# Kernel optimization log

Measured on AMD Instinct MI355X. Metric: run time of the kernel, lower is better.

## Reference

```python
import jax, jax.numpy as jnp
import numpy as np

B, C, H, W = 8, 64, 256, 256  # H must equal W for the second matmul


def setup_inputs() -> dict:
    key = jax.random.key(0)
    kq, kk, kv = jax.random.split(key, 3)
    Q = jax.random.normal(kq, (B, C, H, W), dtype=jnp.float32)
    K = jax.random.normal(kk, (B, C, H, W), dtype=jnp.float32)
    V = jax.random.normal(kv, (B, C, H, W), dtype=jnp.float32)
    di = jnp.ones((1,), dtype=jnp.float32)  # learned scalar scale
    return {"Q": Q, "K": K, "V": V, "di": di}


def reference(Q, K, V, di):
    # similarity[b,c,i,k] = sum_w Q[b,c,i,w] * K[b,c,k,w], scaled by di
    sim = jnp.einsum('bciw,bckw->bcik', Q, K) * di[0]
    attn = jax.nn.softmax(sim, axis=-1)  # [B,C,H,H]
    # residual = attn @ V^T -> [B,C,H,H]; output is residual^T:
    # out[b,c,i,j] = sum_k attn[b,c,j,k] * V[b,c,i,k]
    out = jnp.einsum('bcjk,bcik->bcij', attn, V)
    return out
```

## Files before the change

### kernel.cpp

```cpp
#include <hip/hip_runtime.h>
#include <hip/hip_bf16.h>


typedef __attribute__((ext_vector_type(8))) _Float16 f16x8;
typedef __attribute__((ext_vector_type(4))) float f32x4;
typedef __attribute__((ext_vector_type(16))) float f32x16;

#define BARRIER() asm volatile("s_waitcnt lgkmcnt(0)\n\ts_barrier" ::: "memory")

__device__ __forceinline__ f32x4 mfma16h(f16x8 a, f16x8 b, f32x4 c) {
  return __builtin_amdgcn_mfma_f32_16x16x32_f16(a, b, c, 0, 0, 0);
}
__device__ __forceinline__ f32x16 mfma32h(f16x8 a, f16x8 b, f32x16 c) {
  return __builtin_amdgcn_mfma_f32_32x32x16_f16(a, b, c, 0, 0, 0);
}
__device__ __forceinline__ f16x8 cvt8(f32x4 a, f32x4 b) {
  f16x8 r;
  r[0] = (_Float16)a[0]; r[1] = (_Float16)a[1];
  r[2] = (_Float16)a[2]; r[3] = (_Float16)a[3];
  r[4] = (_Float16)b[0]; r[5] = (_Float16)b[1];
  r[6] = (_Float16)b[2]; r[7] = (_Float16)b[3];
  return r;
}
__device__ __forceinline__ int swz(int row, int byteCol) {
  return row * 512 + (byteCol ^ ((row & 15) << 4));
}

__global__ __launch_bounds__(512, 2) void attn_fused6(
    const float* __restrict__ Q, const float* __restrict__ K,
    const float* __restrict__ V, const float* __restrict__ di,
    float* __restrict__ out) {
  __shared__ short Kbuf[2][32 * 256];
  __shared__ short Abuf[128 * 256];
  short* Vlds = &Kbuf[0][0];

  const int t = threadIdx.x;
  const int lane = t & 63;
  const int wv = t >> 6;
  const int l15 = lane & 15;
  const int l4 = (lane >> 4) & 3;
  const int l31 = lane & 31;
  const int h5 = lane >> 5;

  const int bid = blockIdx.x;
  const int bc = (bid >> 4) * 8 + (bid & 7);
  const int j0 = ((bid >> 3) & 1) << 7;

  const float dival = di[0];
  const size_t base = (size_t)bc << 16;
  const float* Qs = Q + base;
  const float* Ks = K + base;
  const float* Vs = V + base;
  float* Os = out + base;

  const int sr = t >> 4;
  const int sc = (t & 15) << 4;

  f32x4 ka0, ka1, ka2, ka3, kb0, kb1, kb2, kb3;
  {
    const float* p = Ks + sr * 256 + sc;
    ka0 = *(const f32x4*)p;
    ka1 = *(const f32x4*)(p + 4);
    ka2 = *(const f32x4*)(p + 8);
    ka3 = *(const f32x4*)(p + 12);
    const float* q = p + 8192;
    kb0 = *(const f32x4*)q;
    kb1 = *(const f32x4*)(q + 4);
    kb2 = *(const f32x4*)(q + 8);
    kb3 = *(const f32x4*)(q + 12);
  }
  f16x8 qh[8];
  {
    const float* qrow = Qs + (size_t)(j0 + wv * 16 + l15) * 256 + 8 * l4;
#pragma unroll
    for (int s = 0; s < 8; ++s)
      qh[s] = cvt8(*(const f32x4*)(qrow + 32 * s),
                   *(const f32x4*)(qrow + 32 * s + 4));
  }

  f32x4 acc[16];
#pragma unroll
  for (int i = 0; i < 16; ++i) acc[i] = (f32x4){0.f, 0.f, 0.f, 0.f};

#pragma unroll
  for (int ch = 0; ch < 8; ++ch) {
    short* kb = Kbuf[ch & 1];
    if ((ch & 1) == 0) {
      *(f16x8*)((char*)kb + swz(sr, sc * 2)) = cvt8(ka0, ka1);
      *(f16x8*)((char*)kb + swz(sr, sc * 2 + 16)) = cvt8(ka2, ka3);
      if (ch < 6) {
        const float* p = Ks + (ch + 2) * 8192 + sr * 256 + sc;
        ka0 = *(const f32x4*)p;
        ka1 = *(const f32x4*)(p + 4);
        ka2 = *(const f32x4*)(p + 8);
        ka3 = *(const f32x4*)(p + 12);
      }
    } else {
      *(f16x8*)((char*)kb + swz(sr, sc * 2)) = cvt8(kb0, kb1);
      *(f16x8*)((char*)kb + swz(sr, sc * 2 + 16)) = cvt8(kb2, kb3);
      if (ch < 6) {
        const float* p = Ks + (ch + 2) * 8192 + sr * 256 + sc;
        kb0 = *(const f32x4*)p;
        kb1 = *(const f32x4*)(p + 4);
        kb2 = *(const f32x4*)(p + 8);
        kb3 = *(const f32x4*)(p + 12);
      }
    }
    BARRIER();
    __builtin_amdgcn_s_setprio(1);
#pragma unroll
    for (int kf = 0; kf < 2; ++kf) {
      const int kr = kf * 16 + l15;
      f32x4 a = acc[2 * ch + kf];
#pragma unroll
      for (int s = 0; s < 8; ++s) {
        f16x8 bh = *(const f16x8*)((const char*)kb + swz(kr, 64 * s + 16 * l4));
        a = mfma16h(qh[s], bh, a);
      }
      acc[2 * ch + kf] = a;
    }
    __builtin_amdgcn_s_setprio(0);
  }

  const int vr = t >> 3;
  const int vc = (t & 7) << 5;
  f32x4 va[8], vb[8];
  {
    const float* p = Vs + (size_t)vr * 256 + vc;
#pragma unroll
    for (int e = 0; e < 8; ++e) va[e] = *(const f32x4*)(p + 4 * e);
  }

  float mx[4] = {-1e30f, -1e30f, -1e30f, -1e30f};
#pragma unroll
  for (int idx = 0; idx < 16; ++idx)
#pragma unroll
    for (int r = 0; r < 4; ++r) {
      acc[idx][r] *= dival;
      mx[r] = fmaxf(mx[r], acc[idx][r]);
    }
#pragma unroll
  for (int o = 1; o <= 8; o <<= 1)
#pragma unroll
    for (int r = 0; r < 4; ++r) mx[r] = fmaxf(mx[r], __shfl_xor(mx[r], o));
  float sm[4] = {0.f, 0.f, 0.f, 0.f};
#pragma unroll
  for (int idx = 0; idx < 16; ++idx)
#pragma unroll
    for (int r = 0; r < 4; ++r) {
      acc[idx][r] = __expf(acc[idx][r] - mx[r]);
      sm[r] += acc[idx][r];
    }
#pragma unroll
  for (int o = 1; o <= 8; o <<= 1)
#pragma unroll
    for (int r = 0; r < 4; ++r) sm[r] += __shfl_xor(sm[r], o);
#pragma unroll
  for (int r = 0; r < 4; ++r) sm[r] = 1.0f / sm[r];
#pragma unroll
  for (int idx = 0; idx < 16; ++idx)
#pragma unroll
    for (int r = 0; r < 4; ++r) {
      const int row = wv * 16 + 4 * l4 + r;
      *(_Float16*)((char*)Abuf + swz(row, 2 * (idx * 16 + l15))) =
          (_Float16)(acc[idx][r] * sm[r]);
    }
  BARRIER();

  const int ih = wv >> 2;
  const int jg = (wv & 3) * 32;
  f16x8 pb[16];
#pragma unroll
  for (int kk = 0; kk < 16; ++kk)
    pb[kk] =
        *(const f16x8*)((const char*)Abuf + swz(jg + l31, 32 * kk + 16 * h5));

#pragma unroll
  for (int ci = 0; ci < 4; ++ci) {
    if ((ci & 1) == 0) {
#pragma unroll
      for (int e = 0; e < 4; ++e) {
        *(f16x8*)((char*)Vlds + swz(vr, vc * 2 + 16 * e)) =
            cvt8(va[2 * e], va[2 * e + 1]);
      }
      if (ci < 3) {
        const float* p = Vs + (size_t)((ci + 1) * 64 + vr) * 256 + vc;
#pragma unroll
        for (int e = 0; e < 8; ++e) vb[e] = *(const f32x4*)(p + 4 * e);
      }
    } else {
#pragma unroll
      for (int e = 0; e < 4; ++e) {
        *(f16x8*)((char*)Vlds + swz(vr, vc * 2 + 16 * e)) =
            cvt8(vb[2 * e], vb[2 * e + 1]);
      }
      if (ci < 3) {
        const float* p = Vs + (size_t)((ci + 1) * 64 + vr) * 256 + vc;
#pragma unroll
        for (int e = 0; e < 8; ++e) va[e] = *(const f32x4*)(p + 4 * e);
      }
    }
    BARRIER();
    __builtin_amdgcn_s_setprio(1);
    f32x16 o = {};
#pragma unroll
    for (int kk = 0; kk < 16; ++kk) {
      f16x8 vfrag = *(const f16x8*)((const char*)Vlds +
                                    swz(ih * 32 + l31, 32 * kk + 16 * h5));
      o = mfma32h(vfrag, pb[kk], o);
    }
    __builtin_amdgcn_s_setprio(0);
    const int rbase = ci * 64 + ih * 32 + 4 * h5;
    const int col = j0 + jg + l31;
#pragma unroll
    for (int reg = 0; reg < 16; ++reg) {
      const int rw = (reg & 3) + 8 * (reg >> 2);
      Os[(size_t)(rbase + rw) * 256 + col] = o[reg];
    }
    BARRIER();
  }
}

extern "C" void kernel_launch(void* const* d_in, const int* in_sizes, int n_in,
                              void* d_out, int out_size, void* d_ws,
                              size_t ws_size, hipStream_t stream) {
  const float* Q = (const float*)d_in[0];
  const float* K = (const float*)d_in[1];
  const float* V = (const float*)d_in[2];
  const float* di = (const float*)d_in[3];
  float* out = (float*)d_out;
  const int BC = in_sizes[0] / (256 * 256);
  hipLaunchKernelGGL(attn_fused6, dim3(BC * 2), dim3(512), 0, stream, Q, K, V,
                     di, out);
}
```

Measured before the change: 130.1 us.

## Split each block to 64 query rows with cross-wave softmax merge, raise occupancy

Each block now handles 64 output columns instead of 128, so the grid doubles and launch bounds allow 4 blocks per CU. Pairs of waves split the key dimension and combine partial max and sum through a small shared buffer. The second matmul moves from 32x32 to 16x16 MFMA tiles that read the attention matrix straight from LDS. This trades more parallelism and smaller LDS use for loading and converting K and V twice as often per output.

```diff
diff --git a/kernel.cpp b/kernel.cpp
--- a/kernel.cpp
+++ b/kernel.cpp
@@ -4,15 +4,11 @@
 
 typedef __attribute__((ext_vector_type(8))) _Float16 f16x8;
 typedef __attribute__((ext_vector_type(4))) float f32x4;
-typedef __attribute__((ext_vector_type(16))) float f32x16;
 
 #define BARRIER() asm volatile("s_waitcnt lgkmcnt(0)\n\ts_barrier" ::: "memory")
 
 __device__ __forceinline__ f32x4 mfma16h(f16x8 a, f16x8 b, f32x4 c) {
   return __builtin_amdgcn_mfma_f32_16x16x32_f16(a, b, c, 0, 0, 0);
-}
-__device__ __forceinline__ f32x16 mfma32h(f16x8 a, f16x8 b, f32x16 c) {
-  return __builtin_amdgcn_mfma_f32_32x32x16_f16(a, b, c, 0, 0, 0);
 }
 __device__ __forceinline__ f16x8 cvt8(f32x4 a, f32x4 b) {
   f16x8 r;
@@ -26,12 +22,13 @@
   return row * 512 + (byteCol ^ ((row & 15) << 4));
 }
 
-__global__ __launch_bounds__(512, 2) void attn_fused6(
+__global__ __launch_bounds__(512, 4) void attn_fused7(
     const float* __restrict__ Q, const float* __restrict__ K,
     const float* __restrict__ V, const float* __restrict__ di,
     float* __restrict__ out) {
   __shared__ short Kbuf[2][32 * 256];
-  __shared__ short Abuf[128 * 256];
+  __shared__ short Abuf[64 * 256];
+  __shared__ float pmps[64 * 4];
   short* Vlds = &Kbuf[0][0];
 
   const int t = threadIdx.x;
@@ -39,12 +36,10 @@
   const int wv = t >> 6;
   const int l15 = lane & 15;
   const int l4 = (lane >> 4) & 3;
-  const int l31 = lane & 31;
-  const int h5 = lane >> 5;
 
   const int bid = blockIdx.x;
-  const int bc = (bid >> 4) * 8 + (bid & 7);
-  const int j0 = ((bid >> 3) & 1) << 7;
+  const int bc = (bid >> 5) * 8 + (bid & 7);
+  const int j0 = ((bid >> 3) & 3) * 64;
 
   const float dival = di[0];
   const size_t base = (size_t)bc << 16;
@@ -52,6 +47,9 @@
   const float* Ks = K + base;
   const float* Vs = V + base;
   float* Os = out + base;
+
+  const int jt = wv >> 1;
+  const int kt = wv & 1;
 
   const int sr = t >> 4;
   const int sc = (t & 15) << 4;
@@ -71,16 +69,16 @@
   }
   f16x8 qh[8];
   {
-    const float* qrow = Qs + (size_t)(j0 + wv * 16 + l15) * 256 + 8 * l4;
+    const float* qrow = Qs + (size_t)(j0 + 16 * jt + l15) * 256 + 8 * l4;
 #pragma unroll
     for (int s = 0; s < 8; ++s)
       qh[s] = cvt8(*(const f32x4*)(qrow + 32 * s),
                    *(const f32x4*)(qrow + 32 * s + 4));
   }
 
-  f32x4 acc[16];
-#pragma unroll
-  for (int i = 0; i < 16; ++i) acc[i] = (f32x4){0.f, 0.f, 0.f, 0.f};
+  f32x4 acc[8];
+#pragma unroll
+  for (int i = 0; i < 8; ++i) acc[i] = (f32x4){0.f, 0.f, 0.f, 0.f};
 
 #pragma unroll
   for (int ch = 0; ch < 8; ++ch) {
@@ -108,17 +106,14 @@
     }
     BARRIER();
     __builtin_amdgcn_s_setprio(1);
-#pragma unroll
-    for (int kf = 0; kf < 2; ++kf) {
-      const int kr = kf * 16 + l15;
-      f32x4 a = acc[2 * ch + kf];
-#pragma unroll
-      for (int s = 0; s < 8; ++s) {
-        f16x8 bh = *(const f16x8*)((const char*)kb + swz(kr, 64 * s + 16 * l4));
-        a = mfma16h(qh[s], bh, a);
-      }
-      acc[2 * ch + kf] = a;
-    }
+    const int kr = 16 * kt + l15;
+    f32x4 a = acc[ch];
+#pragma unroll
+    for (int s = 0; s < 8; ++s) {
+      f16x8 bh = *(const f16x8*)((const char*)kb + swz(kr, 64 * s + 16 * l4));
+      a = mfma16h(qh[s], bh, a);
+    }
+    acc[ch] = a;
     __builtin_amdgcn_s_setprio(0);
   }
 
@@ -133,11 +128,11 @@
 
   float mx[4] = {-1e30f, -1e30f, -1e30f, -1e30f};
 #pragma unroll
-  for (int idx = 0; idx < 16; ++idx)
-#pragma unroll
-    for (int r = 0; r < 4; ++r) {
-      acc[idx][r] *= dival;
-      mx[r] = fmaxf(mx[r], acc[idx][r]);
+  for (int ch = 0; ch < 8; ++ch)
+#pragma unroll
+    for (int r = 0; r < 4; ++r) {
+      acc[ch][r] *= dival;
+      mx[r] = fmaxf(mx[r], acc[ch][r]);
     }
 #pragma unroll
   for (int o = 1; o <= 8; o <<= 1)
@@ -145,44 +140,50 @@
     for (int r = 0; r < 4; ++r) mx[r] = fmaxf(mx[r], __shfl_xor(mx[r], o));
   float sm[4] = {0.f, 0.f, 0.f, 0.f};
 #pragma unroll
-  for (int idx = 0; idx < 16; ++idx)
-#pragma unroll
-    for (int r = 0; r < 4; ++r) {
-      acc[idx][r] = __expf(acc[idx][r] - mx[r]);
-      sm[r] += acc[idx][r];
+  for (int ch = 0; ch < 8; ++ch)
+#pragma unroll
+    for (int r = 0; r < 4; ++r) {
+      acc[ch][r] = __expf(acc[ch][r] - mx[r]);
+      sm[r] += acc[ch][r];
     }
 #pragma unroll
   for (int o = 1; o <= 8; o <<= 1)
 #pragma unroll
     for (int r = 0; r < 4; ++r) sm[r] += __shfl_xor(sm[r], o);
-#pragma unroll
-  for (int r = 0; r < 4; ++r) sm[r] = 1.0f / sm[r];
-#pragma unroll
-  for (int idx = 0; idx < 16; ++idx)
-#pragma unroll
-    for (int r = 0; r < 4; ++r) {
-      const int row = wv * 16 + 4 * l4 + r;
-      *(_Float16*)((char*)Abuf + swz(row, 2 * (idx * 16 + l15))) =
-          (_Float16)(acc[idx][r] * sm[r]);
-    }
+  if (l15 == 0) {
+#pragma unroll
+    for (int r = 0; r < 4; ++r) {
+      const int row = 16 * jt + 4 * l4 + r;
+      pmps[row * 4 + 2 * kt] = mx[r];
+      pmps[row * 4 + 2 * kt + 1] = sm[r];
+    }
+  }
   BARRIER();
-
-  const int ih = wv >> 2;
-  const int jg = (wv & 3) * 32;
-  f16x8 pb[16];
-#pragma unroll
-  for (int kk = 0; kk < 16; ++kk)
-    pb[kk] =
-        *(const f16x8*)((const char*)Abuf + swz(jg + l31, 32 * kk + 16 * h5));
-
+#pragma unroll
+  for (int r = 0; r < 4; ++r) {
+    const int row = 16 * jt + 4 * l4 + r;
+    f32x4 p = *(const f32x4*)&pmps[row * 4];
+    const float mg = fmaxf(p[0], p[2]);
+    const float Sg = p[1] * __expf(p[0] - mg) + p[3] * __expf(p[2] - mg);
+    const float al = __expf(mx[r] - mg) / Sg;
+#pragma unroll
+    for (int ch = 0; ch < 8; ++ch) {
+      const int col = 32 * ch + 16 * kt + l15;
+      *(_Float16*)((char*)Abuf + swz(row, 2 * col)) =
+          (_Float16)(acc[ch][r] * al);
+    }
+  }
+  BARRIER();
+
+  const int iq = wv >> 1;
+  const int jh = wv & 1;
 #pragma unroll
   for (int ci = 0; ci < 4; ++ci) {
     if ((ci & 1) == 0) {
 #pragma unroll
-      for (int e = 0; e < 4; ++e) {
+      for (int e = 0; e < 4; ++e)
         *(f16x8*)((char*)Vlds + swz(vr, vc * 2 + 16 * e)) =
             cvt8(va[2 * e], va[2 * e + 1]);
-      }
       if (ci < 3) {
         const float* p = Vs + (size_t)((ci + 1) * 64 + vr) * 256 + vc;
 #pragma unroll
@@ -190,10 +191,9 @@
       }
     } else {
 #pragma unroll
-      for (int e = 0; e < 4; ++e) {
+      for (int e = 0; e < 4; ++e)
         *(f16x8*)((char*)Vlds + swz(vr, vc * 2 + 16 * e)) =
             cvt8(vb[2 * e], vb[2 * e + 1]);
-      }
       if (ci < 3) {
         const float* p = Vs + (size_t)((ci + 1) * 64 + vr) * 256 + vc;
 #pragma unroll
@@ -202,20 +202,25 @@
     }
     BARRIER();
     __builtin_amdgcn_s_setprio(1);
-    f32x16 o = {};
-#pragma unroll
-    for (int kk = 0; kk < 16; ++kk) {
+    f32x4 o0 = {0.f, 0.f, 0.f, 0.f}, o1 = {0.f, 0.f, 0.f, 0.f};
+#pragma unroll
+    for (int ks = 0; ks < 8; ++ks) {
       f16x8 vfrag = *(const f16x8*)((const char*)Vlds +
-                                    swz(ih * 32 + l31, 32 * kk + 16 * h5));
-      o = mfma32h(vfrag, pb[kk], o);
+                                    swz(16 * iq + l15, 64 * ks + 16 * l4));
+      f16x8 ab0 = *(const f16x8*)((const char*)Abuf +
+                                  swz(32 * jh + l15, 64 * ks + 16 * l4));
+      f16x8 ab1 = *(const f16x8*)((const char*)Abuf +
+                                  swz(32 * jh + 16 + l15, 64 * ks + 16 * l4));
+      o0 = mfma16h(vfrag, ab0, o0);
+      o1 = mfma16h(vfrag, ab1, o1);
     }
     __builtin_amdgcn_s_setprio(0);
-    const int rbase = ci * 64 + ih * 32 + 4 * h5;
-    const int col = j0 + jg + l31;
-#pragma unroll
-    for (int reg = 0; reg < 16; ++reg) {
-      const int rw = (reg & 3) + 8 * (reg >> 2);
-      Os[(size_t)(rbase + rw) * 256 + col] = o[reg];
+    const int rbase = 64 * ci + 16 * iq + 4 * l4;
+    const int col = j0 + 32 * jh + l15;
+#pragma unroll
+    for (int r = 0; r < 4; ++r) {
+      Os[(size_t)(rbase + r) * 256 + col] = o0[r];
+      Os[(size_t)(rbase + r) * 256 + col + 16] = o1[r];
     }
     BARRIER();
   }
@@ -230,6 +235,6 @@
   const float* di = (const float*)d_in[3];
   float* out = (float*)d_out;
   const int BC = in_sizes[0] / (256 * 256);
-  hipLaunchKernelGGL(attn_fused6, dim3(BC * 2), dim3(512), 0, stream, Q, K, V,
+  hipLaunchKernelGGL(attn_fused7, dim3(BC * 4), dim3(512), 0, stream, Q, K, V,
                      di, out);
 }
```

Result: slower. 185.9 us (+42.9%).

## Shrink LDS staging and register footprint to fit two blocks per CU

Applied to the files above, without the earlier changes.

Halves the K staging tiles (16 rows per chunk over 16 chunks instead of 32 over 8). The V staging is split into half-width column chunks stored in a narrower swizzled layout, so total LDS drops to 80KB. Softmax fragments are read from LDS inside the PV loop rather than held in 16 registers, and launch bounds are raised to favour more resident waves. The aim is to let two 512-thread blocks share a CU and hide memory latency, at the cost of more barriers and more LDS reads per MFMA.

```diff
diff --git a/kernel.cpp b/kernel.cpp
--- a/kernel.cpp
+++ b/kernel.cpp
@@ -22,15 +22,18 @@
   r[6] = (_Float16)b[2]; r[7] = (_Float16)b[3];
   return r;
 }
-__device__ __forceinline__ int swz(int row, int byteCol) {
+__device__ __forceinline__ int swzA(int row, int byteCol) {
   return row * 512 + (byteCol ^ ((row & 15) << 4));
 }
-
-__global__ __launch_bounds__(512, 2) void attn_fused6(
+__device__ __forceinline__ int swzV(int row, int byteCol) {
+  return row * 256 + (byteCol ^ ((row & 15) << 4));
+}
+
+__global__ __launch_bounds__(512, 4) void attn_fused10(
     const float* __restrict__ Q, const float* __restrict__ K,
     const float* __restrict__ V, const float* __restrict__ di,
     float* __restrict__ out) {
-  __shared__ short Kbuf[2][32 * 256];
+  __shared__ short Kbuf[2][16 * 256];
   __shared__ short Abuf[128 * 256];
   short* Vlds = &Kbuf[0][0];
 
@@ -53,25 +56,21 @@
   const float* Vs = V + base;
   float* Os = out + base;
 
-  const int sr = t >> 4;
-  const int sc = (t & 15) << 4;
-
-  f32x4 ka0, ka1, ka2, ka3, kb0, kb1, kb2, kb3;
+  const int sr = t >> 5;
+  const int scb = (t & 31) << 4;
+
+  f32x4 kpA0, kpA1, kpB0, kpB1;
   {
-    const float* p = Ks + sr * 256 + sc;
-    ka0 = *(const f32x4*)p;
-    ka1 = *(const f32x4*)(p + 4);
-    ka2 = *(const f32x4*)(p + 8);
-    ka3 = *(const f32x4*)(p + 12);
-    const float* q = p + 8192;
-    kb0 = *(const f32x4*)q;
-    kb1 = *(const f32x4*)(q + 4);
-    kb2 = *(const f32x4*)(q + 8);
-    kb3 = *(const f32x4*)(q + 12);
+    const float* p = Ks + sr * 256 + (t & 31) * 8;
+    kpA0 = *(const f32x4*)p;
+    kpA1 = *(const f32x4*)(p + 4);
+    const float* q = p + 4096;
+    kpB0 = *(const f32x4*)q;
+    kpB1 = *(const f32x4*)(q + 4);
   }
   f16x8 qh[8];
   {
-    const float* qrow = Qs + (size_t)(j0 + wv * 16 + l15) * 256 + 8 * l4;
+    const float* qrow = Qs + (size_t)(j0 + 16 * wv + l15) * 256 + 8 * l4;
 #pragma unroll
     for (int s = 0; s < 8; ++s)
       qh[s] = cvt8(*(const f32x4*)(qrow + 32 * s),
@@ -83,52 +82,46 @@
   for (int i = 0; i < 16; ++i) acc[i] = (f32x4){0.f, 0.f, 0.f, 0.f};
 
 #pragma unroll
-  for (int ch = 0; ch < 8; ++ch) {
+  for (int ch = 0; ch < 16; ++ch) {
     short* kb = Kbuf[ch & 1];
     if ((ch & 1) == 0) {
-      *(f16x8*)((char*)kb + swz(sr, sc * 2)) = cvt8(ka0, ka1);
-      *(f16x8*)((char*)kb + swz(sr, sc * 2 + 16)) = cvt8(ka2, ka3);
-      if (ch < 6) {
-        const float* p = Ks + (ch + 2) * 8192 + sr * 256 + sc;
-        ka0 = *(const f32x4*)p;
-        ka1 = *(const f32x4*)(p + 4);
-        ka2 = *(const f32x4*)(p + 8);
-        ka3 = *(const f32x4*)(p + 12);
+      *(f16x8*)((char*)kb + swzA(sr, scb)) = cvt8(kpA0, kpA1);
+      BARRIER();
+      if (ch < 14) {
+        const float* p = Ks + (ch + 2) * 4096 + sr * 256 + (t & 31) * 8;
+        kpA0 = *(const f32x4*)p;
+        kpA1 = *(const f32x4*)(p + 4);
       }
     } else {
-      *(f16x8*)((char*)kb + swz(sr, sc * 2)) = cvt8(kb0, kb1);
-      *(f16x8*)((char*)kb + swz(sr, sc * 2 + 16)) = cvt8(kb2, kb3);
-      if (ch < 6) {
-        const float* p = Ks + (ch + 2) * 8192 + sr * 256 + sc;
-        kb0 = *(const f32x4*)p;
-        kb1 = *(const f32x4*)(p + 4);
-        kb2 = *(const f32x4*)(p + 8);
-        kb3 = *(const f32x4*)(p + 12);
-      }
-    }
-    BARRIER();
+      *(f16x8*)((char*)kb + swzA(sr, scb)) = cvt8(kpB0, kpB1);
+      BARRIER();
+      if (ch < 14) {
+        const float* p = Ks + (ch + 2) * 4096 + sr * 256 + (t & 31) * 8;
+        kpB0 = *(const f32x4*)p;
+        kpB1 = *(const f32x4*)(p + 4);
+      }
+    }
     __builtin_amdgcn_s_setprio(1);
-#pragma unroll
-    for (int kf = 0; kf < 2; ++kf) {
-      const int kr = kf * 16 + l15;
-      f32x4 a = acc[2 * ch + kf];
-#pragma unroll
-      for (int s = 0; s < 8; ++s) {
-        f16x8 bh = *(const f16x8*)((const char*)kb + swz(kr, 64 * s + 16 * l4));
-        a = mfma16h(qh[s], bh, a);
-      }
-      acc[2 * ch + kf] = a;
-    }
+    f32x4 a = acc[ch];
+#pragma unroll
+    for (int s = 0; s < 8; ++s) {
+      f16x8 bh = *(const f16x8*)((const char*)kb + swzA(l15, 64 * s + 16 * l4));
+      a = mfma16h(qh[s], bh, a);
+    }
+    acc[ch] = a;
     __builtin_amdgcn_s_setprio(0);
   }
 
   const int vr = t >> 3;
-  const int vc = (t & 7) << 5;
-  f32x4 va[8], vb[8];
+  const int vcf = (t & 7) * 16;
+  f32x4 vpA[4], vpB[4];
   {
-    const float* p = Vs + (size_t)vr * 256 + vc;
-#pragma unroll
-    for (int e = 0; e < 8; ++e) va[e] = *(const f32x4*)(p + 4 * e);
+    const float* p = Vs + (size_t)vr * 256 + vcf;
+#pragma unroll
+    for (int e = 0; e < 4; ++e) vpA[e] = *(const f32x4*)(p + 4 * e);
+    const float* q = p + 128;
+#pragma unroll
+    for (int e = 0; e < 4; ++e) vpB[e] = *(const f32x4*)(q + 4 * e);
   }
 
   float mx[4] = {-1e30f, -1e30f, -1e30f, -1e30f};
@@ -161,61 +154,59 @@
   for (int idx = 0; idx < 16; ++idx)
 #pragma unroll
     for (int r = 0; r < 4; ++r) {
-      const int row = wv * 16 + 4 * l4 + r;
-      *(_Float16*)((char*)Abuf + swz(row, 2 * (idx * 16 + l15))) =
+      const int row = 16 * wv + 4 * l4 + r;
+      *(_Float16*)((char*)Abuf + swzA(row, 2 * (16 * idx + l15))) =
           (_Float16)(acc[idx][r] * sm[r]);
     }
   BARRIER();
 
-  const int ih = wv >> 2;
-  const int jg = (wv & 3) * 32;
-  f16x8 pb[16];
-#pragma unroll
-  for (int kk = 0; kk < 16; ++kk)
-    pb[kk] =
-        *(const f16x8*)((const char*)Abuf + swz(jg + l31, 32 * kk + 16 * h5));
-
-#pragma unroll
-  for (int ci = 0; ci < 4; ++ci) {
-    if ((ci & 1) == 0) {
-#pragma unroll
-      for (int e = 0; e < 4; ++e) {
-        *(f16x8*)((char*)Vlds + swz(vr, vc * 2 + 16 * e)) =
-            cvt8(va[2 * e], va[2 * e + 1]);
-      }
-      if (ci < 3) {
-        const float* p = Vs + (size_t)((ci + 1) * 64 + vr) * 256 + vc;
-#pragma unroll
-        for (int e = 0; e < 8; ++e) vb[e] = *(const f32x4*)(p + 4 * e);
+  const int ig = wv >> 2;
+  const int jg = wv & 3;
+  f32x16 o = {};
+#pragma unroll
+  for (int cc = 0; cc < 8; ++cc) {
+    const int kh = cc & 1;
+    if ((cc & 1) == 0) {
+      *(f16x8*)((char*)Vlds + swzV(vr, 2 * vcf)) = cvt8(vpA[0], vpA[1]);
+      *(f16x8*)((char*)Vlds + swzV(vr, 2 * vcf + 16)) = cvt8(vpA[2], vpA[3]);
+      BARRIER();
+      if (cc < 6) {
+        const float* p =
+            Vs + (size_t)(64 * ((cc + 2) >> 1) + vr) * 256 + vcf;
+#pragma unroll
+        for (int e = 0; e < 4; ++e) vpA[e] = *(const f32x4*)(p + 4 * e);
       }
     } else {
-#pragma unroll
-      for (int e = 0; e < 4; ++e) {
-        *(f16x8*)((char*)Vlds + swz(vr, vc * 2 + 16 * e)) =
-            cvt8(vb[2 * e], vb[2 * e + 1]);
-      }
-      if (ci < 3) {
-        const float* p = Vs + (size_t)((ci + 1) * 64 + vr) * 256 + vc;
-#pragma unroll
-        for (int e = 0; e < 8; ++e) va[e] = *(const f32x4*)(p + 4 * e);
-      }
-    }
-    BARRIER();
+      *(f16x8*)((char*)Vlds + swzV(vr, 2 * vcf)) = cvt8(vpB[0], vpB[1]);
+      *(f16x8*)((char*)Vlds + swzV(vr, 2 * vcf + 16)) = cvt8(vpB[2], vpB[3]);
+      BARRIER();
+      if (cc < 6) {
+        const float* p =
+            Vs + (size_t)(64 * ((cc + 2) >> 1) + vr) * 256 + 128 + vcf;
+#pragma unroll
+        for (int e = 0; e < 4; ++e) vpB[e] = *(const f32x4*)(p + 4 * e);
+      }
+    }
     __builtin_amdgcn_s_setprio(1);
-    f32x16 o = {};
-#pragma unroll
-    for (int kk = 0; kk < 16; ++kk) {
+#pragma unroll
+    for (int kk = 0; kk < 8; ++kk) {
       f16x8 vfrag = *(const f16x8*)((const char*)Vlds +
-                                    swz(ih * 32 + l31, 32 * kk + 16 * h5));
-      o = mfma32h(vfrag, pb[kk], o);
+                                    swzV(32 * ig + l31, 32 * kk + 16 * h5));
+      f16x8 pfrag =
+          *(const f16x8*)((const char*)Abuf +
+                          swzA(32 * jg + l31, 256 * kh + 32 * kk + 16 * h5));
+      o = mfma32h(vfrag, pfrag, o);
     }
     __builtin_amdgcn_s_setprio(0);
-    const int rbase = ci * 64 + ih * 32 + 4 * h5;
-    const int col = j0 + jg + l31;
-#pragma unroll
-    for (int reg = 0; reg < 16; ++reg) {
-      const int rw = (reg & 3) + 8 * (reg >> 2);
-      Os[(size_t)(rbase + rw) * 256 + col] = o[reg];
+    if (kh == 1) {
+      const int rbase = 64 * (cc >> 1) + 32 * ig + 4 * h5;
+      const int col = j0 + 32 * jg + l31;
+#pragma unroll
+      for (int reg = 0; reg < 16; ++reg) {
+        const int rw = (reg & 3) + 8 * (reg >> 2);
+        Os[(size_t)(rbase + rw) * 256 + col] = o[reg];
+      }
+      o = (f32x16){};
     }
     BARRIER();
   }
@@ -230,6 +221,6 @@
   const float* di = (const float*)d_in[3];
   float* out = (float*)d_out;
   const int BC = in_sizes[0] / (256 * 256);
-  hipLaunchKernelGGL(attn_fused6, dim3(BC * 2), dim3(512), 0, stream, Q, K, V,
+  hipLaunchKernelGGL(attn_fused10, dim3(BC * 2), dim3(512), 0, stream, Q, K, V,
                      di, out);
 }
```

Result: faster. 112.2 us (-13.8%).
